# Kernel tuning notes

Measured on AMD Instinct MI355X. Metric: run time of the kernel, lower is better.

The kernel has to match this reference:

```python
import jax, jax.numpy as jnp
import numpy as np

N, D_IN, D_H, D_OUT, M = 256, 768, 768, 512, 100000


def setup_inputs() -> dict:
    key = jax.random.key(0)
    ks = jax.random.split(key, 8)
    img_feats = jax.random.normal(ks[0], (N, D_IN), dtype=jnp.float32)
    w1 = jax.random.normal(ks[1], (D_H, D_IN), dtype=jnp.float32) * (1.0 / np.sqrt(D_IN))
    b1 = jax.random.normal(ks[2], (D_H,), dtype=jnp.float32) * 0.01
    w2 = jax.random.normal(ks[3], (D_OUT, D_H), dtype=jnp.float32) * (1.0 / np.sqrt(D_H))
    b2 = jax.random.normal(ks[4], (D_OUT,), dtype=jnp.float32) * 0.01
    logit_scale = jnp.asarray(np.log(1.0 / 0.07), dtype=jnp.float32)
    loc = jax.random.normal(ks[5], (M, D_OUT), dtype=jnp.float32)
    loc_feats = loc / jnp.linalg.norm(loc, axis=1, keepdims=True)  # pre-normalized gallery
    gps_gallery = jax.random.uniform(ks[6], (M, 2), dtype=jnp.float32, minval=-90.0, maxval=90.0)
    return {
        "img_feats": img_feats, "w1": w1, "b1": b1, "w2": w2, "b2": b2,
        "logit_scale": logit_scale, "loc_feats": loc_feats,
        "gps_gallery": gps_gallery, "top_k": 5,
    }


def reference(img_feats, w1, b1, w2, b2, logit_scale, loc_feats, gps_gallery, top_k):
    # Tsfm MLP head: Linear -> ReLU -> Linear
    h = jax.nn.relu(img_feats @ w1.T + b1)            # [N, D_H]
    img = h @ w2.T + b2                               # [N, D_OUT]
    # F.normalize(dim=1)
    img_n = img / jnp.linalg.norm(img, axis=1, keepdims=True)
    # forward_cached: scaled cosine-similarity logits against 100K gallery
    logits = jnp.exp(logit_scale) * (img_n @ loc_feats.T)  # [N, M]
    # predict: softmax over full gallery row, then top-k retrieval
    probs = jax.nn.softmax(logits, axis=-1)
    top_vals, top_idx = jax.lax.top_k(probs, top_k)   # [N, k]
    top_pred_gps = gps_gallery[top_idx[0]]            # [k, 2] (first image, as in original)
    top_pred_prob = top_vals[0]                       # [k]
    return (logits, top_pred_gps, top_pred_prob)
```

## Files before the change

### kernel.cpp

```cpp
#include <hip/hip_runtime.h>
#include <math.h>

#define N_IMG 256
#define DIN   768
#define DH    768
#define DOUT  512
#define M_GAL 100000
#define CAP   2048
#define MT    1568

typedef __bf16 bf16_t;
typedef __bf16 bf16x8 __attribute__((ext_vector_type(8)));
typedef float  f32x4  __attribute__((ext_vector_type(4)));
typedef float  f32x16 __attribute__((ext_vector_type(16)));

#define OFF_H      0
#define OFF_IMG    (N_IMG*DH)
#define OFF_IMGN   (OFF_IMG  + N_IMG*DOUT)
#define OFF_IMGT   (OFF_IMGN + N_IMG*DOUT)
#define OFF_STATS  (OFF_IMGT + N_IMG*DOUT/2)
#define OFF_CIDX   (OFF_STATS + 4)
#define OFF_CVAL   (OFF_CIDX + CAP)

#define OUT_GPS  ((size_t)N_IMG * (size_t)M_GAL)
#define OUT_PROB (OUT_GPS + 10)

__device__ inline unsigned fkey(float x) {
  unsigned u = __float_as_uint(x);
  return (u & 0x80000000u) ? ~u : (u | 0x80000000u);
}
__device__ inline float fkey_inv(unsigned k) {
  unsigned u = (k & 0x80000000u) ? (k ^ 0x80000000u) : ~k;
  return __uint_as_float(u);
}

template<int KDIM, int NCOLS, bool RELU>
__global__ __launch_bounds__(256) void mlp_gemm(const float* __restrict__ A,
    const float* __restrict__ B, const float* __restrict__ bias,
    float* __restrict__ C, unsigned* stats_init) {
  if (stats_init && blockIdx.x == 0 && blockIdx.y == 0 && threadIdx.x == 0) {
    stats_init[0] = 0u; stats_init[1] = 0u; stats_init[2] = 0u;
  }
  __shared__ float As[32][34];
  __shared__ float Bs[32][34];
  const int t  = threadIdx.x;
  const int rowbase = blockIdx.y * 32;
  const int colbase = blockIdx.x * 32;
  const int sm = t >> 3;
  const int kc = (t & 7) << 2;
  const int ty = t >> 4, tx = t & 15;
  float a00 = 0.f, a01 = 0.f, a10 = 0.f, a11 = 0.f;
  for (int kt = 0; kt < KDIM; kt += 32) {
    float4 av = *(const float4*)(A + (size_t)(rowbase + sm) * KDIM + kt + kc);
    float4 bv = *(const float4*)(B + (size_t)(colbase + sm) * KDIM + kt + kc);
    __syncthreads();
    As[kc+0][sm] = av.x; As[kc+1][sm] = av.y; As[kc+2][sm] = av.z; As[kc+3][sm] = av.w;
    Bs[kc+0][sm] = bv.x; Bs[kc+1][sm] = bv.y; Bs[kc+2][sm] = bv.z; Bs[kc+3][sm] = bv.w;
    __syncthreads();
#pragma unroll
    for (int j = 0; j < 32; ++j) {
      float2 a = *(const float2*)(&As[j][2*ty]);
      float2 b = *(const float2*)(&Bs[j][2*tx]);
      a00 = fmaf(a.x, b.x, a00); a01 = fmaf(a.x, b.y, a01);
      a10 = fmaf(a.y, b.x, a10); a11 = fmaf(a.y, b.y, a11);
    }
  }
  const int r0 = rowbase + 2*ty;
  const int c0 = colbase + 2*tx;
  const float bb0 = bias[c0], bb1 = bias[c0+1];
  float v00 = a00 + bb0, v01 = a01 + bb1, v10 = a10 + bb0, v11 = a11 + bb1;
  if (RELU) {
    v00 = fmaxf(v00, 0.f); v01 = fmaxf(v01, 0.f);
    v10 = fmaxf(v10, 0.f); v11 = fmaxf(v11, 0.f);
  }
  C[(size_t)r0*NCOLS + c0]       = v00; C[(size_t)r0*NCOLS + c0 + 1]     = v01;
  C[(size_t)(r0+1)*NCOLS + c0]   = v10; C[(size_t)(r0+1)*NCOLS + c0 + 1] = v11;
}

__global__ __launch_bounds__(256) void norm_cast_kernel(const float* __restrict__ img,
    float* __restrict__ img_n, bf16_t* __restrict__ img_t) {
  const int row = blockIdx.x, t = threadIdx.x;
  const float v0 = img[row*DOUT + t];
  const float v1 = img[row*DOUT + 256 + t];
  float s = v0*v0 + v1*v1;
  for (int o = 32; o > 0; o >>= 1) s += __shfl_down(s, o);
  __shared__ float ws4[4];
  if ((t & 63) == 0) ws4[t >> 6] = s;
  __syncthreads();
  const float tot = ws4[0] + ws4[1] + ws4[2] + ws4[3];
  const float inv = 1.0f / sqrtf(tot);
  const float n0 = v0 * inv, n1 = v1 * inv;
  img_n[row*DOUT + t]       = n0;
  img_n[row*DOUT + 256 + t] = n1;
  const int k0 = t, k1 = t + 256;
  img_t[(((k0 >> 3)*N_IMG) + row)*8 + (k0 & 7)] = (bf16_t)n0;
  img_t[(((k1 >> 3)*N_IMG) + row)*8 + (k1 & 7)] = (bf16_t)n1;
}

__global__ __launch_bounds__(256, 4) void logits_kernel(const float* __restrict__ loc,
    const bf16_t* __restrict__ img_t, const float* __restrict__ ls,
    float* __restrict__ out, float* __restrict__ sumexp, unsigned* __restrict__ maxkey) {
  __shared__ bf16_t Asl[8 * 256 * 8];
  const int t = threadIdx.x;
  const int w = t >> 6, l = t & 63;
  const int wr = w >> 1;
  const int wc = w & 1;
  const int hi = l >> 5;
  const int lo = l & 31;
  const int mb = blockIdx.x * 64;
  const int m  = mb + wc * 32 + lo;
  const int mc = m < M_GAL ? m : (M_GAL - 1);
  const float* bp = loc + (size_t)mc * 512 + hi * 8;

  f32x16 acc[4];
#pragma unroll
  for (int i = 0; i < 4; ++i) acc[i] = (f32x16)(0.f);

  float4 B0[3], B1[3];

#define ISSUE(kt) {                                                   \
    const int s_ = (kt) % 3;                                          \
    const float* p_ = bp + (kt) * 16;                                 \
    B0[s_] = *(const float4*)p_;                                      \
    B1[s_] = *(const float4*)(p_ + 4);                                \
  }

#define COMPUTE(kt) {                                                 \
    const int s_  = (kt) % 3;                                         \
    const int kl_ = ((kt) & 3) * 2 + hi;         \
    bf16x8 af_[4];                                                    \
    _Pragma("unroll")                                                 \
    for (int i_ = 0; i_ < 4; ++i_)                                    \
      af_[i_] = *(const bf16x8*)(Asl + (kl_ * 256 + wr * 128 + i_ * 32 + lo) * 8); \
    bf16x8 bf_;                                                       \
    bf_[0] = (bf16_t)B0[s_].x; bf_[1] = (bf16_t)B0[s_].y;             \
    bf_[2] = (bf16_t)B0[s_].z; bf_[3] = (bf16_t)B0[s_].w;             \
    bf_[4] = (bf16_t)B1[s_].x; bf_[5] = (bf16_t)B1[s_].y;             \
    bf_[6] = (bf16_t)B1[s_].z; bf_[7] = (bf16_t)B1[s_].w;             \
    _Pragma("unroll")                                                 \
    for (int i_ = 0; i_ < 4; ++i_)                                    \
      acc[i_] = __builtin_amdgcn_mfma_f32_32x32x16_bf16(af_[i_], bf_, acc[i_], 0, 0, 0); \
  }

#define STAGE(c_) {                                                   \
    _Pragma("unroll")                                                 \
    for (int r_ = 0; r_ < 8; ++r_) {                                  \
      __builtin_amdgcn_global_load_lds(                               \
          (__attribute__((address_space(1))) void*)(img_t + (((c_) * 8 + r_) * 256 + t) * 8), \
          (__attribute__((address_space(3))) void*)(Asl + (r_ * 256 + t) * 8), \
          16, 0, 0);                                                  \
    } }

  ISSUE(0); ISSUE(1);
  STAGE(0);
  __syncthreads();

#pragma unroll
  for (int c = 0; c < 8; ++c) {
#pragma unroll
    for (int q = 0; q < 4; ++q) {
      const int kt = c * 4 + q;
      if (kt + 2 < 32) { ISSUE(kt + 2); }
      COMPUTE(kt);
    }
    if (c < 7) {
      __syncthreads();
      STAGE(c + 1);
      __syncthreads();
    }
  }
#undef ISSUE
#undef COMPUTE
#undef STAGE

  const float scale = expf(ls[0]);
  if (wr == 0) {
    float mx = -1e30f, se = 0.f;
    if (hi == 0 && m < M_GAL) {
      const float v = scale * acc[0][0];
      mx = v;
      se = expf(v);
    }
#pragma unroll
    for (int o = 1; o < 64; o <<= 1) {
      mx = fmaxf(mx, __shfl_xor(mx, o));
      se += __shfl_xor(se, o);
    }
    if (l == 0) { atomicAdd(sumexp, se); atomicMax(maxkey, fkey(mx)); }
  }
  if (m < M_GAL) {
#pragma unroll
    for (int i = 0; i < 4; ++i) {
      const int ib = wr * 128 + i * 32 + hi * 4;
#pragma unroll
      for (int r = 0; r < 16; ++r) {
        const int img = ib + (r & 3) + 8 * (r >> 2);
        out[(size_t)img * M_GAL + m] = scale * acc[i][r];
      }
    }
  }
}

__global__ __launch_bounds__(256) void collect_kernel(const float* __restrict__ out,
    const unsigned* __restrict__ maxkey, unsigned* __restrict__ counter,
    int* __restrict__ cidx) {
  const int i = blockIdx.x * 256 + threadIdx.x;
  if (i >= M_GAL) return;
  const float thresh = fkey_inv(*maxkey) - 0.8f;
  if (out[i] > thresh) {
    const unsigned p = atomicAdd(counter, 1u);
    if (p < CAP) cidx[p] = i;
  }
}

__global__ __launch_bounds__(256) void recompute_kernel(const float* __restrict__ loc,
    const float* __restrict__ img_n, const float* __restrict__ ls,
    const unsigned* __restrict__ counter, const int* __restrict__ cidx,
    float* __restrict__ cval) {
  const int w = threadIdx.x >> 6, l = threadIdx.x & 63;
  const unsigned cnt = *counter;
  const int n = (int)(cnt < CAP ? cnt : CAP);
  const float scale = expf(ls[0]);
  for (int c = blockIdx.x * 4 + w; c < n; c += gridDim.x * 4) {
    const int idx = cidx[c];
    const float* B = loc + (size_t)idx * 512;
    float s = 0.f;
#pragma unroll
    for (int e = 0; e < 8; ++e) s = fmaf(img_n[l + e*64], B[l + e*64], s);
    for (int o = 32; o > 0; o >>= 1) s += __shfl_down(s, o);
    if (l == 0) cval[c] = scale * s;
  }
}

__global__ __launch_bounds__(256) void finalize_kernel(const unsigned* __restrict__ counter,
    const int* __restrict__ cidx, const float* __restrict__ cval,
    const float* __restrict__ gps, const float* __restrict__ sumexp,
    float* __restrict__ out) {
  __shared__ float v[CAP];
  __shared__ int   id[CAP];
  __shared__ float rv[256];
  __shared__ int   ri[256];
  __shared__ int   rs[256];
  const int t = threadIdx.x;
  const unsigned cnt = *counter;
  const int n = (int)(cnt < CAP ? cnt : CAP);
  for (int i = t; i < CAP; i += 256) {
    v[i]  = (i < n) ? cval[i] : -1e30f;
    id[i] = (i < n) ? cidx[i] : 0x7fffffff;
  }
  const float se = *sumexp;
  __syncthreads();
  for (int k = 0; k < 5; ++k) {
    float bv = -1e30f; int bidx = 0x7fffffff; int bslot = -1;
    for (int i = t; i < CAP; i += 256) {
      const float vi = v[i]; const int ii = id[i];
      if (vi > bv || (vi == bv && ii < bidx)) { bv = vi; bidx = ii; bslot = i; }
    }
    rv[t] = bv; ri[t] = bidx; rs[t] = bslot;
    __syncthreads();
    for (int s = 128; s > 0; s >>= 1) {
      if (t < s) {
        if (rv[t+s] > rv[t] || (rv[t+s] == rv[t] && ri[t+s] < ri[t])) {
          rv[t] = rv[t+s]; ri[t] = ri[t+s]; rs[t] = rs[t+s];
        }
      }
      __syncthreads();
    }
    if (t == 0) {
      const int sl = rs[0]; const int gi = ri[0]; const float lv = rv[0];
      float g0 = 0.f, g1 = 0.f, pr = 0.f;
      if (sl >= 0 && gi != 0x7fffffff) {
        g0 = gps[(size_t)gi*2]; g1 = gps[(size_t)gi*2 + 1];
        pr = expf(lv) / se;
        v[sl] = -1e30f; id[sl] = 0x7fffffff;
      }
      out[OUT_GPS + 2*k]     = g0;
      out[OUT_GPS + 2*k + 1] = g1;
      out[OUT_PROB + k]      = pr;
    }
    __syncthreads();
  }
}

extern "C" void kernel_launch(void* const* d_in, const int* in_sizes, int n_in,
                              void* d_out, int out_size, void* d_ws, size_t ws_size,
                              hipStream_t stream) {
  const float* img_feats = (const float*)d_in[0];
  const float* w1  = (const float*)d_in[1];
  const float* b1  = (const float*)d_in[2];
  const float* w2  = (const float*)d_in[3];
  const float* b2  = (const float*)d_in[4];
  const float* ls  = (const float*)d_in[5];
  const float* loc = (const float*)d_in[6];
  const float* gps = (const float*)d_in[7];
  float* out = (float*)d_out;
  float* ws  = (float*)d_ws;

  float*    h       = ws + OFF_H;
  float*    img     = ws + OFF_IMG;
  float*    img_n   = ws + OFF_IMGN;
  bf16_t*   img_t   = (bf16_t*)(ws + OFF_IMGT);
  float*    sumexp  = ws + OFF_STATS;
  unsigned* maxkey  = (unsigned*)(ws + OFF_STATS + 1);
  unsigned* counter = (unsigned*)(ws + OFF_STATS + 2);
  int*      cidx    = (int*)(ws + OFF_CIDX);
  float*    cval    = ws + OFF_CVAL;

  mlp_gemm<DIN, DH, true><<<dim3(DH/32, N_IMG/32), 256, 0, stream>>>(
      img_feats, w1, b1, h, (unsigned*)(ws + OFF_STATS));
  mlp_gemm<DH, DOUT, false><<<dim3(DOUT/32, N_IMG/32), 256, 0, stream>>>(
      h, w2, b2, img, nullptr);
  norm_cast_kernel<<<N_IMG, 256, 0, stream>>>(img, img_n, img_t);
  logits_kernel<<<MT, 256, 0, stream>>>(loc, img_t, ls, out, sumexp, maxkey);
  collect_kernel<<<(M_GAL + 255) / 256, 256, 0, stream>>>(out, maxkey, counter, cidx);
  recompute_kernel<<<128, 256, 0, stream>>>(loc, img_n, ls, counter, cidx, cval);
  finalize_kernel<<<1, 256, 0, stream>>>(counter, cidx, cval, gps, sumexp, out);
}
```

Measured before the change: 452.7 us.

## Stage gallery tile through LDS with coalesced loads instead of per-lane strided reads

The gallery (B operand) is now loaded cooperatively, with 8 consecutive threads reading one 256-byte row chunk per stage. It is converted to bf16 and written to a new LDS buffer, and the MFMA B fragments are then read from LDS. Previously each lane read two float4s per k-step directly from global memory with a row stride of 2 KB, which coalesces poorly. This also removes the duplicate B loads that both wave-rows issued for the same columns. The cost is extra LDS traffic, more LDS per block (which may limit occupancy), and a per-chunk register prefetch instead of the previous 2-step-deep register pipeline.

```diff
diff --git a/kernel.cpp b/kernel.cpp
--- a/kernel.cpp
+++ b/kernel.cpp
@@ -101,6 +101,7 @@
     const bf16_t* __restrict__ img_t, const float* __restrict__ ls,
     float* __restrict__ out, float* __restrict__ sumexp, unsigned* __restrict__ maxkey) {
   __shared__ bf16_t Asl[8 * 256 * 8];
+  __shared__ bf16_t Bsl[8 * 64 * 8];
   const int t = threadIdx.x;
   const int w = t >> 6, l = t & 63;
   const int wr = w >> 1;
@@ -109,40 +110,43 @@
   const int lo = l & 31;
   const int mb = blockIdx.x * 64;
   const int m  = mb + wc * 32 + lo;
-  const int mc = m < M_GAL ? m : (M_GAL - 1);
-  const float* bp = loc + (size_t)mc * 512 + hi * 8;
+
+  const int sk8 = t & 7, sr0 = t >> 3;
+  const int gr0 = min(mb + sr0,      M_GAL - 1);
+  const int gr1 = min(mb + 32 + sr0, M_GAL - 1);
+  const float* sp0 = loc + (size_t)gr0 * 512 + sk8 * 8;
+  const float* sp1 = loc + (size_t)gr1 * 512 + sk8 * 8;
+  bf16_t* bw0 = Bsl + (sk8 * 64 + sr0) * 8;
+  bf16_t* bw1 = bw0 + 32 * 8;
 
   f32x16 acc[4];
 #pragma unroll
   for (int i = 0; i < 4; ++i) acc[i] = (f32x16)(0.f);
 
-  float4 B0[3], B1[3];
-
-#define ISSUE(kt) {                                                   \
-    const int s_ = (kt) % 3;                                          \
-    const float* p_ = bp + (kt) * 16;                                 \
-    B0[s_] = *(const float4*)p_;                                      \
-    B1[s_] = *(const float4*)(p_ + 4);                                \
-  }
-
-#define COMPUTE(kt) {                                                 \
-    const int s_  = (kt) % 3;                                         \
-    const int kl_ = ((kt) & 3) * 2 + hi;         \
-    bf16x8 af_[4];                                                    \
-    _Pragma("unroll")                                                 \
-    for (int i_ = 0; i_ < 4; ++i_)                                    \
-      af_[i_] = *(const bf16x8*)(Asl + (kl_ * 256 + wr * 128 + i_ * 32 + lo) * 8); \
-    bf16x8 bf_;                                                       \
-    bf_[0] = (bf16_t)B0[s_].x; bf_[1] = (bf16_t)B0[s_].y;             \
-    bf_[2] = (bf16_t)B0[s_].z; bf_[3] = (bf16_t)B0[s_].w;             \
-    bf_[4] = (bf16_t)B1[s_].x; bf_[5] = (bf16_t)B1[s_].y;             \
-    bf_[6] = (bf16_t)B1[s_].z; bf_[7] = (bf16_t)B1[s_].w;             \
-    _Pragma("unroll")                                                 \
-    for (int i_ = 0; i_ < 4; ++i_)                                    \
-      acc[i_] = __builtin_amdgcn_mfma_f32_32x32x16_bf16(af_[i_], bf_, acc[i_], 0, 0, 0); \
-  }
-
-#define STAGE(c_) {                                                   \
+  float4 r00, r01, r10, r11;
+
+#define BLOAD(c_) {                                                   \
+    const float* p0_ = sp0 + (c_) * 64;                               \
+    const float* p1_ = sp1 + (c_) * 64;                               \
+    r00 = *(const float4*)p0_; r01 = *(const float4*)(p0_ + 4);       \
+    r10 = *(const float4*)p1_; r11 = *(const float4*)(p1_ + 4);       \
+  }
+
+#define BWRITE() {                                                    \
+    bf16x8 b0_, b1_;                                                  \
+    b0_[0] = (bf16_t)r00.x; b0_[1] = (bf16_t)r00.y;                   \
+    b0_[2] = (bf16_t)r00.z; b0_[3] = (bf16_t)r00.w;                   \
+    b0_[4] = (bf16_t)r01.x; b0_[5] = (bf16_t)r01.y;                   \
+    b0_[6] = (bf16_t)r01.z; b0_[7] = (bf16_t)r01.w;                   \
+    b1_[0] = (bf16_t)r10.x; b1_[1] = (bf16_t)r10.y;                   \
+    b1_[2] = (bf16_t)r10.z; b1_[3] = (bf16_t)r10.w;                   \
+    b1_[4] = (bf16_t)r11.x; b1_[5] = (bf16_t)r11.y;                   \
+    b1_[6] = (bf16_t)r11.z; b1_[7] = (bf16_t)r11.w;                   \
+    *(bf16x8*)bw0 = b0_;                                              \
+    *(bf16x8*)bw1 = b1_;                                              \
+  }
+
+#define STAGEA(c_) {                                                  \
     _Pragma("unroll")                                                 \
     for (int r_ = 0; r_ < 8; ++r_) {                                  \
       __builtin_amdgcn_global_load_lds(                               \
@@ -151,27 +155,41 @@
           16, 0, 0);                                                  \
     } }
 
-  ISSUE(0); ISSUE(1);
-  STAGE(0);
+#define COMPUTE(kt) {                                                 \
+    const int kl_ = ((kt) & 3) * 2 + hi;         \
+    bf16x8 af_[4];                                                    \
+    _Pragma("unroll")                                                 \
+    for (int i_ = 0; i_ < 4; ++i_)                                    \
+      af_[i_] = *(const bf16x8*)(Asl + (kl_ * 256 + wr * 128 + i_ * 32 + lo) * 8); \
+    const bf16x8 bf_ = *(const bf16x8*)(Bsl + (kl_ * 64 + wc * 32 + lo) * 8); \
+    _Pragma("unroll")                                                 \
+    for (int i_ = 0; i_ < 4; ++i_)                                    \
+      acc[i_] = __builtin_amdgcn_mfma_f32_32x32x16_bf16(af_[i_], bf_, acc[i_], 0, 0, 0); \
+  }
+
+  BLOAD(0);
+  STAGEA(0);
+  BWRITE();
   __syncthreads();
 
 #pragma unroll
   for (int c = 0; c < 8; ++c) {
+    if (c < 7) { BLOAD(c + 1); }
 #pragma unroll
     for (int q = 0; q < 4; ++q) {
-      const int kt = c * 4 + q;
-      if (kt + 2 < 32) { ISSUE(kt + 2); }
-      COMPUTE(kt);
+      COMPUTE(c * 4 + q);
     }
     if (c < 7) {
       __syncthreads();
-      STAGE(c + 1);
+      STAGEA(c + 1);
+      BWRITE();
       __syncthreads();
     }
   }
-#undef ISSUE
+#undef BLOAD
+#undef BWRITE
+#undef STAGEA
 #undef COMPUTE
-#undef STAGE
 
   const float scale = expf(ls[0]);
   if (wr == 0) {
```

Measured after the change: 442.1 us. 1.02x faster.
